# Kernel optimization log

Measured on AMD Instinct MI355X. Metric: run time of the kernel, lower is better.

Reference implementation:

```python
import jax, jax.numpy as jnp
import numpy as np
from jax import lax

NUM_ITER = 20
EPS = 1e-8

# Sobel stencils (match torch grad_x / grad_y exactly)
SX = jnp.array([[-1., 0., 1.], [-2., 0., 2.], [-1., 0., 1.]], jnp.float32)
SY = jnp.array([[-1., -2., -1.], [0., 0., 0.], [1., 2., 1.]], jnp.float32)


def _conv(x, w, groups=1):
    # x: [B,C,H,W], w: [O, C//groups, kh, kw]; cross-correlation, SAME pad (= torch Conv2d padding=1)
    return lax.conv_general_dilated(x, w, (1, 1), 'SAME',
                                    feature_group_count=groups,
                                    dimension_numbers=('NCHW', 'OIHW', 'NCHW'))


def setup_inputs() -> dict:
    key = jax.random.key(0)
    k1, = jax.random.split(key, 1)
    x = jax.random.uniform(k1, (4, 2, 256, 256), dtype=jnp.float32)
    return {
        'x': x,
        'lambda_': jnp.array([0.15], jnp.float32),
        'tau': jnp.array([0.25], jnp.float32),
        'theta': jnp.array([0.3], jnp.float32),
    }


def reference(x, lambda_, tau, theta):
    B, _, H, W = x.shape
    grad_w = jnp.stack([SX, SY])[:, None]            # [2,1,3,3] -> 2-channel image gradient
    sx_dw = jnp.broadcast_to(SX, (2, 1, 3, 3))       # depthwise Sobel-x on 2-channel p
    sy_dw = jnp.broadcast_to(SY, (2, 1, 3, 3))       # depthwise Sobel-y on 2-channel p

    im1 = x[:, 1:2]                                  # [B,1,H,W]
    rho_c = im1 - x[:, 0:1]                          # temporal difference
    grad_im = _conv(im1, grad_w)                     # [B,2,H,W] spatial gradient of frame 1
    norm_grad = jnp.sum(grad_im * grad_im, axis=1, keepdims=True) + EPS  # [B,1,H,W]

    r = tau / theta                                  # [1]
    zeros = jnp.zeros((B, 2, H, W), x.dtype)

    def step(carry, _):
        u, p1, p2 = carry
        rho = rho_c + jnp.sum(grad_im * u, axis=1, keepdims=True)
        th = theta * lambda_ * norm_grad
        # thresholding step (TV-L1 data term prox)
        v = u - jnp.where(jnp.abs(rho) < th,
                          rho / norm_grad,
                          theta * lambda_ * jnp.sign(rho)) * grad_im
        # u update with divergence-like term (original uses 3x3 Sobel gradx/grady on p)
        u = v + theta * (_conv(p1, sx_dw, groups=2) + _conv(p2, sy_dw, groups=2))
        gradu1 = _conv(u[:, 0:1], grad_w)            # [B,2,H,W]
        gradu2 = _conv(u[:, 1:2], grad_w)
        p1 = (p1 + r * gradu1) / (1.0 + r * jnp.sum(jnp.abs(gradu1), axis=1, keepdims=True))
        p2 = (p2 + r * gradu2) / (1.0 + r * jnp.sum(jnp.abs(gradu2), axis=1, keepdims=True))
        return (u, p1, p2), None

    (u, _, _), _ = lax.scan(step, (zeros, zeros, zeros), None, length=NUM_ITER)
    return u
```

## Files before the change

### kernel.cpp

```cpp
#include <hip/hip_runtime.h>

#define HH 256
#define WW 256
#define BB 4
#define HW (HH*WW)
#define N_ITER 20
#define EPSV 1e-8f

#define FUSE 4
#define TILE 32
#define HALO (2*FUSE)
#define EXT  (TILE + 2*HALO)
#define EPAD 49
#define NTHR 768
#define RPS  3

__device__ __forceinline__ float ldz(const float* __restrict__ p, int y, int x) {
    if ((unsigned)y < HH && (unsigned)x < WW) return p[y*WW + x];
    return 0.0f;
}

template<int FIRST, int LAST>
__global__ __launch_bounds__(NTHR)
void tvl1_fused(const float* __restrict__ xin,
                float* __restrict__ u,
                float* __restrict__ p1, float* __restrict__ p2,
                float* __restrict__ gxc, float* __restrict__ gyc,
                float* __restrict__ rcc,
                const float* __restrict__ lam, const float* __restrict__ tau,
                const float* __restrict__ the) {
    __shared__ float4 su[EXT][EPAD];
    __shared__ float4 sp[EXT][EPAD];

    const int tid = threadIdx.x;
    const int sx  = tid % EXT;
    const int sy3 = (tid / EXT) * RPS;
    const int b  = blockIdx.z;
    const int ox = blockIdx.x*TILE - HALO;
    const int oy = blockIdx.y*TILE - HALO;
    const int pb = b*2*HW, cb = b*HW;
    const float theta = the[0];
    const float tl = theta * lam[0];
    const float r = tau[0] / theta;

    const int gxx = ox + sx;
    const bool inx = ((unsigned)gxx < WW);

    float ru0[RPS], ru1[RPS], rp10[RPS], rp11[RPS], rp20[RPS], rp21[RPS];
    float rgx[RPS], rgy[RPS], rrc[RPS];
    bool updr[RPS];

    const int rT = (sy3 == 0) ? 0 : sy3 - 1;
    const int rB = (sy3 + RPS >= EXT) ? EXT-1 : sy3 + RPS;
    const int xm = (sx == 0) ? 0 : sx - 1;
    const int xp = (sx == EXT-1) ? EXT-1 : sx + 1;

    #pragma unroll
    for (int j = 0; j < RPS; ++j) {
        int ry = sy3 + j;
        int gyy = oy + ry;
        bool img = inx && ((unsigned)gyy < HH);
        updr[j] = img && (ry >= 1) && (ry < EXT-1) && (sx >= 1) && (sx < EXT-1);
    }

    if (FIRST) {
        float im1r[RPS], im0r[RPS];
        #pragma unroll
        for (int j = 0; j < RPS; ++j) {
            int gyy = oy + sy3 + j;
            im1r[j] = ldz(xin + pb + HW, gyy, gxx);
            im0r[j] = ldz(xin + pb,      gyy, gxx);
            su[sy3 + j][sx] = make_float4(im1r[j], im0r[j], 0.f, 0.f);
        }
        __syncthreads();
        {
            float4 Vm[RPS+2], Vc[RPS+2], Vp[RPS+2];
            Vm[0] = su[rT][xm];     Vc[0] = su[rT][sx];   Vp[0] = su[rT][xp];
            Vm[1] = su[sy3  ][xm];                        Vp[1] = su[sy3  ][xp];
            Vm[2] = su[sy3+1][xm];                        Vp[2] = su[sy3+1][xp];
            Vm[3] = su[sy3+2][xm];                        Vp[3] = su[sy3+2][xp];
            Vm[4] = su[rB][xm];     Vc[4] = su[rB][sx];   Vp[4] = su[rB][xp];
            Vc[1] = make_float4(im1r[0], im0r[0], 0.f, 0.f);
            Vc[2] = make_float4(im1r[1], im0r[1], 0.f, 0.f);
            Vc[3] = make_float4(im1r[2], im0r[2], 0.f, 0.f);
            #pragma unroll
            for (int j = 0; j < RPS; ++j) {
                rgx[j] = (Vp[j].x-Vm[j].x) + 2.f*(Vp[j+1].x-Vm[j+1].x) + (Vp[j+2].x-Vm[j+2].x);
                rgy[j] = (Vm[j+2].x-Vm[j].x) + 2.f*(Vc[j+2].x-Vc[j].x) + (Vp[j+2].x-Vp[j].x);
                rrc[j] = im1r[j] - im0r[j];
                ru0[j]=0.f; ru1[j]=0.f;
                rp10[j]=0.f; rp11[j]=0.f; rp20[j]=0.f; rp21[j]=0.f;
                int ry = sy3 + j;
                if (ry >= HALO && ry < HALO+TILE && sx >= HALO && sx < HALO+TILE) {
                    int gi = (oy + ry)*WW + gxx;
                    gxc[cb + gi] = rgx[j];
                    gyc[cb + gi] = rgy[j];
                    rcc[cb + gi] = rrc[j];
                }
            }
        }
        __syncthreads();
        #pragma unroll
        for (int j = 0; j < RPS; ++j) {
            su[sy3 + j][sx] = make_float4(0.f, 0.f, 0.f, 0.f);
            sp[sy3 + j][sx] = make_float4(0.f, 0.f, 0.f, 0.f);
        }
        __syncthreads();
    } else {
        #pragma unroll
        for (int j = 0; j < RPS; ++j) {
            int ry = sy3 + j;
            int gyy = oy + ry;
            bool img = inx && ((unsigned)gyy < HH);
            float v0=0.f,v1=0.f,w0=0.f,w1=0.f,w2=0.f,w3=0.f,a=0.f,c=0.f,d=0.f;
            if (img) {
                int gi = gyy*WW + gxx;
                v0 = u[pb + gi];   v1 = u[pb + HW + gi];
                w0 = p1[pb + gi];  w1 = p1[pb + HW + gi];
                w2 = p2[pb + gi];  w3 = p2[pb + HW + gi];
                a  = gxc[cb + gi]; c  = gyc[cb + gi];  d = rcc[cb + gi];
            }
            ru0[j]=v0; ru1[j]=v1; rp10[j]=w0; rp11[j]=w1; rp20[j]=w2; rp21[j]=w3;
            rgx[j]=a; rgy[j]=c; rrc[j]=d;
            su[ry][sx] = make_float4(v0, v1, 0.f, 0.f);
            sp[ry][sx] = make_float4(w0, w1, w2, w3);
        }
        __syncthreads();
    }

    #pragma unroll
    for (int it = 0; it < FUSE; ++it) {
        {
            float4 Wm[RPS+2], Wc[RPS+2], Wp[RPS+2];
            Wm[0] = sp[rT][xm];     Wc[0] = sp[rT][sx];   Wp[0] = sp[rT][xp];
            Wm[1] = sp[sy3  ][xm];                        Wp[1] = sp[sy3  ][xp];
            Wm[2] = sp[sy3+1][xm];                        Wp[2] = sp[sy3+1][xp];
            Wm[3] = sp[sy3+2][xm];                        Wp[3] = sp[sy3+2][xp];
            Wm[4] = sp[rB][xm];     Wc[4] = sp[rB][sx];   Wp[4] = sp[rB][xp];
            Wc[1] = make_float4(rp10[0], rp11[0], rp20[0], rp21[0]);
            Wc[2] = make_float4(rp10[1], rp11[1], rp20[1], rp21[1]);
            Wc[3] = make_float4(rp10[2], rp11[2], rp20[2], rp21[2]);
            #pragma unroll
            for (int j = 0; j < RPS; ++j) {
                if (updr[j]) {
                    float x0 = (Wp[j].x-Wm[j].x) + 2.f*(Wp[j+1].x-Wm[j+1].x) + (Wp[j+2].x-Wm[j+2].x);
                    float x1 = (Wp[j].y-Wm[j].y) + 2.f*(Wp[j+1].y-Wm[j+1].y) + (Wp[j+2].y-Wm[j+2].y);
                    float y0 = (Wm[j+2].z-Wm[j].z) + 2.f*(Wc[j+2].z-Wc[j].z) + (Wp[j+2].z-Wp[j].z);
                    float y1 = (Wm[j+2].w-Wm[j].w) + 2.f*(Wc[j+2].w-Wc[j].w) + (Wp[j+2].w-Wp[j].w);

                    float g_x = rgx[j], g_y = rgy[j];
                    float ng  = g_x*g_x + g_y*g_y + EPSV;
                    float rho = rrc[j] + g_x*ru0[j] + g_y*ru1[j];
                    float th  = tl * ng;
                    float sgn = (rho > 0.f) ? 1.f : ((rho < 0.f) ? -1.f : 0.f);
                    float dd  = (fabsf(rho) < th) ? (rho / ng) : (tl * sgn);
                    ru0[j] = ru0[j] - dd*g_x + theta*(x0 + y0);
                    ru1[j] = ru1[j] - dd*g_y + theta*(x1 + y1);
                    su[sy3+j][sx] = make_float4(ru0[j], ru1[j], 0.f, 0.f);
                }
            }
        }
        __syncthreads();

        if (LAST && it == FUSE-1) break;

        {
            float4 Vm[RPS+2], Vc[RPS+2], Vp[RPS+2];
            Vm[0] = su[rT][xm];     Vc[0] = su[rT][sx];   Vp[0] = su[rT][xp];
            Vm[1] = su[sy3  ][xm];                        Vp[1] = su[sy3  ][xp];
            Vm[2] = su[sy3+1][xm];                        Vp[2] = su[sy3+1][xp];
            Vm[3] = su[sy3+2][xm];                        Vp[3] = su[sy3+2][xp];
            Vm[4] = su[rB][xm];     Vc[4] = su[rB][sx];   Vp[4] = su[rB][xp];
            Vc[1] = make_float4(ru0[0], ru1[0], 0.f, 0.f);
            Vc[2] = make_float4(ru0[1], ru1[1], 0.f, 0.f);
            Vc[3] = make_float4(ru0[2], ru1[2], 0.f, 0.f);
            #pragma unroll
            for (int j = 0; j < RPS; ++j) {
                if (updr[j]) {
                    float g1x = (Vp[j].x-Vm[j].x) + 2.f*(Vp[j+1].x-Vm[j+1].x) + (Vp[j+2].x-Vm[j+2].x);
                    float g1y = (Vm[j+2].x-Vm[j].x) + 2.f*(Vc[j+2].x-Vc[j].x) + (Vp[j+2].x-Vp[j].x);
                    float g2x = (Vp[j].y-Vm[j].y) + 2.f*(Vp[j+1].y-Vm[j+1].y) + (Vp[j+2].y-Vm[j+2].y);
                    float g2y = (Vm[j+2].y-Vm[j].y) + 2.f*(Vc[j+2].y-Vc[j].y) + (Vp[j+2].y-Vp[j].y);
                    float inv1 = 1.f / (1.f + r*(fabsf(g1x) + fabsf(g1y)));
                    float inv2 = 1.f / (1.f + r*(fabsf(g2x) + fabsf(g2y)));
                    rp10[j] = (rp10[j] + r*g1x) * inv1;
                    rp11[j] = (rp11[j] + r*g1y) * inv1;
                    rp20[j] = (rp20[j] + r*g2x) * inv2;
                    rp21[j] = (rp21[j] + r*g2y) * inv2;
                    sp[sy3+j][sx] = make_float4(rp10[j], rp11[j], rp20[j], rp21[j]);
                }
            }
        }
        __syncthreads();
    }

    #pragma unroll
    for (int j = 0; j < RPS; ++j) {
        int ry = sy3 + j;
        if (updr[j] && ry >= HALO && ry < HALO+TILE && sx >= HALO && sx < HALO+TILE) {
            int go = (oy + ry)*WW + (ox + sx);
            u[pb + go]      = ru0[j];
            u[pb + HW + go] = ru1[j];
            if (!LAST) {
                p1[pb + go]      = rp10[j];
                p1[pb + HW + go] = rp11[j];
                p2[pb + go]      = rp20[j];
                p2[pb + HW + go] = rp21[j];
            }
        }
    }
}

extern "C" void kernel_launch(void* const* d_in, const int* in_sizes, int n_in,
                              void* d_out, int out_size, void* d_ws, size_t ws_size,
                              hipStream_t stream) {
    const float* xin = (const float*)d_in[0];
    const float* lam = (const float*)d_in[1];
    const float* tau = (const float*)d_in[2];
    const float* the = (const float*)d_in[3];
    float* u = (float*)d_out;

    float* ws = (float*)d_ws;
    float* p1 = ws;
    float* p2 = ws + (size_t)BB*2*HW;
    float* gx = ws + (size_t)2*BB*2*HW;
    float* gy = gx + (size_t)BB*HW;
    float* rc = gy + (size_t)BB*HW;

    dim3 blk(NTHR, 1, 1);
    dim3 grd(WW/TILE, HH/TILE, BB);
    tvl1_fused<1,0><<<grd, blk, 0, stream>>>(xin, u, p1, p2, gx, gy, rc, lam, tau, the);
    tvl1_fused<0,0><<<grd, blk, 0, stream>>>(xin, u, p1, p2, gx, gy, rc, lam, tau, the);
    tvl1_fused<0,0><<<grd, blk, 0, stream>>>(xin, u, p1, p2, gx, gy, rc, lam, tau, the);
    tvl1_fused<0,0><<<grd, blk, 0, stream>>>(xin, u, p1, p2, gx, gy, rc, lam, tau, the);
    tvl1_fused<0,1><<<grd, blk, 0, stream>>>(xin, u, p1, p2, gx, gy, rc, lam, tau, the);
}
```

Measured before the change: 91.15 us.

## Replace five kernel launches with one cooperative persistent kernel using grid sync

Measured after the change: 244.2 us. 168% more time.

```diff
diff --git a/kernel.cpp b/kernel.cpp
--- a/kernel.cpp
+++ b/kernel.cpp
@@ -1,4 +1,7 @@
 #include <hip/hip_runtime.h>
+#include <hip/hip_cooperative_groups.h>
+
+namespace cg = cooperative_groups;
 
 #define HH 256
 #define WW 256
@@ -8,6 +11,7 @@
 #define EPSV 1e-8f
 
 #define FUSE 4
+#define NPH  5
 #define TILE 32
 #define HALO (2*FUSE)
 #define EXT  (TILE + 2*HALO)
@@ -20,15 +24,14 @@
     return 0.0f;
 }
 
-template<int FIRST, int LAST>
 __global__ __launch_bounds__(NTHR)
-void tvl1_fused(const float* __restrict__ xin,
-                float* __restrict__ u,
-                float* __restrict__ p1, float* __restrict__ p2,
-                float* __restrict__ gxc, float* __restrict__ gyc,
-                float* __restrict__ rcc,
-                const float* __restrict__ lam, const float* __restrict__ tau,
-                const float* __restrict__ the) {
+void tvl1_persist(const float* __restrict__ xin,
+                  float* __restrict__ u,
+                  float* __restrict__ p1, float* __restrict__ p2,
+                  const float* __restrict__ lam, const float* __restrict__ tau,
+                  const float* __restrict__ the) {
+    cg::grid_group gridg = cg::this_grid();
+
     __shared__ float4 su[EXT][EPAD];
     __shared__ float4 sp[EXT][EPAD];
 
@@ -38,7 +41,7 @@
     const int b  = blockIdx.z;
     const int ox = blockIdx.x*TILE - HALO;
     const int oy = blockIdx.y*TILE - HALO;
-    const int pb = b*2*HW, cb = b*HW;
+    const int pb = b*2*HW;
     const float theta = the[0];
     const float tl = theta * lam[0];
     const float r = tau[0] / theta;
@@ -58,12 +61,11 @@
     #pragma unroll
     for (int j = 0; j < RPS; ++j) {
         int ry = sy3 + j;
-        int gyy = oy + ry;
-        bool img = inx && ((unsigned)gyy < HH);
+        bool img = inx && ((unsigned)(oy + ry) < HH);
         updr[j] = img && (ry >= 1) && (ry < EXT-1) && (sx >= 1) && (sx < EXT-1);
     }
 
-    if (FIRST) {
+    {
         float im1r[RPS], im0r[RPS];
         #pragma unroll
         for (int j = 0; j < RPS; ++j) {
@@ -73,141 +75,138 @@
             su[sy3 + j][sx] = make_float4(im1r[j], im0r[j], 0.f, 0.f);
         }
         __syncthreads();
-        {
-            float4 Vm[RPS+2], Vc[RPS+2], Vp[RPS+2];
-            Vm[0] = su[rT][xm];     Vc[0] = su[rT][sx];   Vp[0] = su[rT][xp];
-            Vm[1] = su[sy3  ][xm];                        Vp[1] = su[sy3  ][xp];
-            Vm[2] = su[sy3+1][xm];                        Vp[2] = su[sy3+1][xp];
-            Vm[3] = su[sy3+2][xm];                        Vp[3] = su[sy3+2][xp];
-            Vm[4] = su[rB][xm];     Vc[4] = su[rB][sx];   Vp[4] = su[rB][xp];
-            Vc[1] = make_float4(im1r[0], im0r[0], 0.f, 0.f);
-            Vc[2] = make_float4(im1r[1], im0r[1], 0.f, 0.f);
-            Vc[3] = make_float4(im1r[2], im0r[2], 0.f, 0.f);
+        float4 Vm[RPS+2], Vc[RPS+2], Vp[RPS+2];
+        Vm[0] = su[rT][xm];     Vc[0] = su[rT][sx];   Vp[0] = su[rT][xp];
+        Vm[1] = su[sy3  ][xm];                        Vp[1] = su[sy3  ][xp];
+        Vm[2] = su[sy3+1][xm];                        Vp[2] = su[sy3+1][xp];
+        Vm[3] = su[sy3+2][xm];                        Vp[3] = su[sy3+2][xp];
+        Vm[4] = su[rB][xm];     Vc[4] = su[rB][sx];   Vp[4] = su[rB][xp];
+        Vc[1] = make_float4(im1r[0], im0r[0], 0.f, 0.f);
+        Vc[2] = make_float4(im1r[1], im0r[1], 0.f, 0.f);
+        Vc[3] = make_float4(im1r[2], im0r[2], 0.f, 0.f);
+        #pragma unroll
+        for (int j = 0; j < RPS; ++j) {
+            rgx[j] = (Vp[j].x-Vm[j].x) + 2.f*(Vp[j+1].x-Vm[j+1].x) + (Vp[j+2].x-Vm[j+2].x);
+            rgy[j] = (Vm[j+2].x-Vm[j].x) + 2.f*(Vc[j+2].x-Vc[j].x) + (Vp[j+2].x-Vp[j].x);
+            rrc[j] = im1r[j] - im0r[j];
+            ru0[j]=0.f; ru1[j]=0.f;
+            rp10[j]=0.f; rp11[j]=0.f; rp20[j]=0.f; rp21[j]=0.f;
+        }
+        __syncthreads();
+        #pragma unroll
+        for (int j = 0; j < RPS; ++j) {
+            su[sy3 + j][sx] = make_float4(0.f, 0.f, 0.f, 0.f);
+            sp[sy3 + j][sx] = make_float4(0.f, 0.f, 0.f, 0.f);
+        }
+        __syncthreads();
+    }
+
+    for (int ph = 0; ph < NPH; ++ph) {
+        const bool last = (ph == NPH-1);
+
+        if (ph > 0) {
             #pragma unroll
             for (int j = 0; j < RPS; ++j) {
-                rgx[j] = (Vp[j].x-Vm[j].x) + 2.f*(Vp[j+1].x-Vm[j+1].x) + (Vp[j+2].x-Vm[j+2].x);
-                rgy[j] = (Vm[j+2].x-Vm[j].x) + 2.f*(Vc[j+2].x-Vc[j].x) + (Vp[j+2].x-Vp[j].x);
-                rrc[j] = im1r[j] - im0r[j];
-                ru0[j]=0.f; ru1[j]=0.f;
-                rp10[j]=0.f; rp11[j]=0.f; rp20[j]=0.f; rp21[j]=0.f;
                 int ry = sy3 + j;
-                if (ry >= HALO && ry < HALO+TILE && sx >= HALO && sx < HALO+TILE) {
-                    int gi = (oy + ry)*WW + gxx;
-                    gxc[cb + gi] = rgx[j];
-                    gyc[cb + gi] = rgy[j];
-                    rcc[cb + gi] = rrc[j];
-                }
-            }
-        }
-        __syncthreads();
-        #pragma unroll
-        for (int j = 0; j < RPS; ++j) {
-            su[sy3 + j][sx] = make_float4(0.f, 0.f, 0.f, 0.f);
-            sp[sy3 + j][sx] = make_float4(0.f, 0.f, 0.f, 0.f);
-        }
-        __syncthreads();
-    } else {
+                int gyy = oy + ry;
+                bool img = inx && ((unsigned)gyy < HH);
+                float v0=0.f,v1=0.f,w0=0.f,w1=0.f,w2=0.f,w3=0.f;
+                if (img) {
+                    int gi = gyy*WW + gxx;
+                    v0 = u[pb + gi];   v1 = u[pb + HW + gi];
+                    w0 = p1[pb + gi];  w1 = p1[pb + HW + gi];
+                    w2 = p2[pb + gi];  w3 = p2[pb + HW + gi];
+                }
+                ru0[j]=v0; ru1[j]=v1; rp10[j]=w0; rp11[j]=w1; rp20[j]=w2; rp21[j]=w3;
+                su[ry][sx] = make_float4(v0, v1, 0.f, 0.f);
+                sp[ry][sx] = make_float4(w0, w1, w2, w3);
+            }
+            __syncthreads();
+        }
+
+        #pragma unroll
+        for (int it = 0; it < FUSE; ++it) {
+            {
+                float4 Wm[RPS+2], Wc[RPS+2], Wp[RPS+2];
+                Wm[0] = sp[rT][xm];     Wc[0] = sp[rT][sx];   Wp[0] = sp[rT][xp];
+                Wm[1] = sp[sy3  ][xm];                        Wp[1] = sp[sy3  ][xp];
+                Wm[2] = sp[sy3+1][xm];                        Wp[2] = sp[sy3+1][xp];
+                Wm[3] = sp[sy3+2][xm];                        Wp[3] = sp[sy3+2][xp];
+                Wm[4] = sp[rB][xm];     Wc[4] = sp[rB][sx];   Wp[4] = sp[rB][xp];
+                Wc[1] = make_float4(rp10[0], rp11[0], rp20[0], rp21[0]);
+                Wc[2] = make_float4(rp10[1], rp11[1], rp20[1], rp21[1]);
+                Wc[3] = make_float4(rp10[2], rp11[2], rp20[2], rp21[2]);
+                #pragma unroll
+                for (int j = 0; j < RPS; ++j) {
+                    if (updr[j]) {
+                        float x0 = (Wp[j].x-Wm[j].x) + 2.f*(Wp[j+1].x-Wm[j+1].x) + (Wp[j+2].x-Wm[j+2].x);
+                        float x1 = (Wp[j].y-Wm[j].y) + 2.f*(Wp[j+1].y-Wm[j+1].y) + (Wp[j+2].y-Wm[j+2].y);
+                        float y0 = (Wm[j+2].z-Wm[j].z) + 2.f*(Wc[j+2].z-Wc[j].z) + (Wp[j+2].z-Wp[j].z);
+                        float y1 = (Wm[j+2].w-Wm[j].w) + 2.f*(Wc[j+2].w-Wc[j].w) + (Wp[j+2].w-Wp[j].w);
+
+                        float g_x = rgx[j], g_y = rgy[j];
+                        float ng  = g_x*g_x + g_y*g_y + EPSV;
+                        float rho = rrc[j] + g_x*ru0[j] + g_y*ru1[j];
+                        float th  = tl * ng;
+                        float sgn = (rho > 0.f) ? 1.f : ((rho < 0.f) ? -1.f : 0.f);
+                        float dd  = (fabsf(rho) < th) ? (rho / ng) : (tl * sgn);
+                        ru0[j] = ru0[j] - dd*g_x + theta*(x0 + y0);
+                        ru1[j] = ru1[j] - dd*g_y + theta*(x1 + y1);
+                        su[sy3+j][sx] = make_float4(ru0[j], ru1[j], 0.f, 0.f);
+                    }
+                }
+            }
+            __syncthreads();
+
+            if (last && it == FUSE-1) break;
+
+            {
+                float4 Vm[RPS+2], Vc[RPS+2], Vp[RPS+2];
+                Vm[0] = su[rT][xm];     Vc[0] = su[rT][sx];   Vp[0] = su[rT][xp];
+                Vm[1] = su[sy3  ][xm];                        Vp[1] = su[sy3  ][xp];
+                Vm[2] = su[sy3+1][xm];                        Vp[2] = su[sy3+1][xp];
+                Vm[3] = su[sy3+2][xm];                        Vp[3] = su[sy3+2][xp];
+                Vm[4] = su[rB][xm];     Vc[4] = su[rB][sx];   Vp[4] = su[rB][xp];
+                Vc[1] = make_float4(ru0[0], ru1[0], 0.f, 0.f);
+                Vc[2] = make_float4(ru0[1], ru1[1], 0.f, 0.f);
+                Vc[3] = make_float4(ru0[2], ru1[2], 0.f, 0.f);
+                #pragma unroll
+                for (int j = 0; j < RPS; ++j) {
+                    if (updr[j]) {
+                        float g1x = (Vp[j].x-Vm[j].x) + 2.f*(Vp[j+1].x-Vm[j+1].x) + (Vp[j+2].x-Vm[j+2].x);
+                        float g1y = (Vm[j+2].x-Vm[j].x) + 2.f*(Vc[j+2].x-Vc[j].x) + (Vp[j+2].x-Vp[j].x);
+                        float g2x = (Vp[j].y-Vm[j].y) + 2.f*(Vp[j+1].y-Vm[j+1].y) + (Vp[j+2].y-Vm[j+2].y);
+                        float g2y = (Vm[j+2].y-Vm[j].y) + 2.f*(Vc[j+2].y-Vc[j].y) + (Vp[j+2].y-Vp[j].y);
+                        float inv1 = 1.f / (1.f + r*(fabsf(g1x) + fabsf(g1y)));
+                        float inv2 = 1.f / (1.f + r*(fabsf(g2x) + fabsf(g2y)));
+                        rp10[j] = (rp10[j] + r*g1x) * inv1;
+                        rp11[j] = (rp11[j] + r*g1y) * inv1;
+                        rp20[j] = (rp20[j] + r*g2x) * inv2;
+                        rp21[j] = (rp21[j] + r*g2y) * inv2;
+                        sp[sy3+j][sx] = make_float4(rp10[j], rp11[j], rp20[j], rp21[j]);
+                    }
+                }
+            }
+            __syncthreads();
+        }
+
         #pragma unroll
         for (int j = 0; j < RPS; ++j) {
             int ry = sy3 + j;
-            int gyy = oy + ry;
-            bool img = inx && ((unsigned)gyy < HH);
-            float v0=0.f,v1=0.f,w0=0.f,w1=0.f,w2=0.f,w3=0.f,a=0.f,c=0.f,d=0.f;
-            if (img) {
-                int gi = gyy*WW + gxx;
-                v0 = u[pb + gi];   v1 = u[pb + HW + gi];
-                w0 = p1[pb + gi];  w1 = p1[pb + HW + gi];
-                w2 = p2[pb + gi];  w3 = p2[pb + HW + gi];
-                a  = gxc[cb + gi]; c  = gyc[cb + gi];  d = rcc[cb + gi];
-            }
-            ru0[j]=v0; ru1[j]=v1; rp10[j]=w0; rp11[j]=w1; rp20[j]=w2; rp21[j]=w3;
-            rgx[j]=a; rgy[j]=c; rrc[j]=d;
-            su[ry][sx] = make_float4(v0, v1, 0.f, 0.f);
-            sp[ry][sx] = make_float4(w0, w1, w2, w3);
-        }
-        __syncthreads();
-    }
-
-    #pragma unroll
-    for (int it = 0; it < FUSE; ++it) {
-        {
-            float4 Wm[RPS+2], Wc[RPS+2], Wp[RPS+2];
-            Wm[0] = sp[rT][xm];     Wc[0] = sp[rT][sx];   Wp[0] = sp[rT][xp];
-            Wm[1] = sp[sy3  ][xm];                        Wp[1] = sp[sy3  ][xp];
-            Wm[2] = sp[sy3+1][xm];                        Wp[2] = sp[sy3+1][xp];
-            Wm[3] = sp[sy3+2][xm];                        Wp[3] = sp[sy3+2][xp];
-            Wm[4] = sp[rB][xm];     Wc[4] = sp[rB][sx];   Wp[4] = sp[rB][xp];
-            Wc[1] = make_float4(rp10[0], rp11[0], rp20[0], rp21[0]);
-            Wc[2] = make_float4(rp10[1], rp11[1], rp20[1], rp21[1]);
-            Wc[3] = make_float4(rp10[2], rp11[2], rp20[2], rp21[2]);
-            #pragma unroll
-            for (int j = 0; j < RPS; ++j) {
-                if (updr[j]) {
-                    float x0 = (Wp[j].x-Wm[j].x) + 2.f*(Wp[j+1].x-Wm[j+1].x) + (Wp[j+2].x-Wm[j+2].x);
-                    float x1 = (Wp[j].y-Wm[j].y) + 2.f*(Wp[j+1].y-Wm[j+1].y) + (Wp[j+2].y-Wm[j+2].y);
-                    float y0 = (Wm[j+2].z-Wm[j].z) + 2.f*(Wc[j+2].z-Wc[j].z) + (Wp[j+2].z-Wp[j].z);
-                    float y1 = (Wm[j+2].w-Wm[j].w) + 2.f*(Wc[j+2].w-Wc[j].w) + (Wp[j+2].w-Wp[j].w);
-
-                    float g_x = rgx[j], g_y = rgy[j];
-                    float ng  = g_x*g_x + g_y*g_y + EPSV;
-                    float rho = rrc[j] + g_x*ru0[j] + g_y*ru1[j];
-                    float th  = tl * ng;
-                    float sgn = (rho > 0.f) ? 1.f : ((rho < 0.f) ? -1.f : 0.f);
-                    float dd  = (fabsf(rho) < th) ? (rho / ng) : (tl * sgn);
-                    ru0[j] = ru0[j] - dd*g_x + theta*(x0 + y0);
-                    ru1[j] = ru1[j] - dd*g_y + theta*(x1 + y1);
-                    su[sy3+j][sx] = make_float4(ru0[j], ru1[j], 0.f, 0.f);
-                }
-            }
-        }
-        __syncthreads();
-
-        if (LAST && it == FUSE-1) break;
-
-        {
-            float4 Vm[RPS+2], Vc[RPS+2], Vp[RPS+2];
-            Vm[0] = su[rT][xm];     Vc[0] = su[rT][sx];   Vp[0] = su[rT][xp];
-            Vm[1] = su[sy3  ][xm];                        Vp[1] = su[sy3  ][xp];
-            Vm[2] = su[sy3+1][xm];                        Vp[2] = su[sy3+1][xp];
-            Vm[3] = su[sy3+2][xm];                        Vp[3] = su[sy3+2][xp];
-            Vm[4] = su[rB][xm];     Vc[4] = su[rB][sx];   Vp[4] = su[rB][xp];
-            Vc[1] = make_float4(ru0[0], ru1[0], 0.f, 0.f);
-            Vc[2] = make_float4(ru0[1], ru1[1], 0.f, 0.f);
-            Vc[3] = make_float4(ru0[2], ru1[2], 0.f, 0.f);
-            #pragma unroll
-            for (int j = 0; j < RPS; ++j) {
-                if (updr[j]) {
-                    float g1x = (Vp[j].x-Vm[j].x) + 2.f*(Vp[j+1].x-Vm[j+1].x) + (Vp[j+2].x-Vm[j+2].x);
-                    float g1y = (Vm[j+2].x-Vm[j].x) + 2.f*(Vc[j+2].x-Vc[j].x) + (Vp[j+2].x-Vp[j].x);
-                    float g2x = (Vp[j].y-Vm[j].y) + 2.f*(Vp[j+1].y-Vm[j+1].y) + (Vp[j+2].y-Vm[j+2].y);
-                    float g2y = (Vm[j+2].y-Vm[j].y) + 2.f*(Vc[j+2].y-Vc[j].y) + (Vp[j+2].y-Vp[j].y);
-                    float inv1 = 1.f / (1.f + r*(fabsf(g1x) + fabsf(g1y)));
-                    float inv2 = 1.f / (1.f + r*(fabsf(g2x) + fabsf(g2y)));
-                    rp10[j] = (rp10[j] + r*g1x) * inv1;
-                    rp11[j] = (rp11[j] + r*g1y) * inv1;
-                    rp20[j] = (rp20[j] + r*g2x) * inv2;
-                    rp21[j] = (rp21[j] + r*g2y) * inv2;
-                    sp[sy3+j][sx] = make_float4(rp10[j], rp11[j], rp20[j], rp21[j]);
-                }
-            }
-        }
-        __syncthreads();
-    }
-
-    #pragma unroll
-    for (int j = 0; j < RPS; ++j) {
-        int ry = sy3 + j;
-        if (updr[j] && ry >= HALO && ry < HALO+TILE && sx >= HALO && sx < HALO+TILE) {
-            int go = (oy + ry)*WW + (ox + sx);
-            u[pb + go]      = ru0[j];
-            u[pb + HW + go] = ru1[j];
-            if (!LAST) {
-                p1[pb + go]      = rp10[j];
-                p1[pb + HW + go] = rp11[j];
-                p2[pb + go]      = rp20[j];
-                p2[pb + HW + go] = rp21[j];
-            }
-        }
+            if (updr[j] && ry >= HALO && ry < HALO+TILE && sx >= HALO && sx < HALO+TILE) {
+                int go = (oy + ry)*WW + (ox + sx);
+                u[pb + go]      = ru0[j];
+                u[pb + HW + go] = ru1[j];
+                if (!last) {
+                    p1[pb + go]      = rp10[j];
+                    p1[pb + HW + go] = rp11[j];
+                    p2[pb + go]      = rp20[j];
+                    p2[pb + HW + go] = rp21[j];
+                }
+            }
+        }
+
+        if (!last) gridg.sync();
     }
 }
 
@@ -223,15 +222,11 @@
     float* ws = (float*)d_ws;
     float* p1 = ws;
     float* p2 = ws + (size_t)BB*2*HW;
-    float* gx = ws + (size_t)2*BB*2*HW;
-    float* gy = gx + (size_t)BB*HW;
-    float* rc = gy + (size_t)BB*HW;
 
     dim3 blk(NTHR, 1, 1);
     dim3 grd(WW/TILE, HH/TILE, BB);
-    tvl1_fused<1,0><<<grd, blk, 0, stream>>>(xin, u, p1, p2, gx, gy, rc, lam, tau, the);
-    tvl1_fused<0,0><<<grd, blk, 0, stream>>>(xin, u, p1, p2, gx, gy, rc, lam, tau, the);
-    tvl1_fused<0,0><<<grd, blk, 0, stream>>>(xin, u, p1, p2, gx, gy, rc, lam, tau, the);
-    tvl1_fused<0,0><<<grd, blk, 0, stream>>>(xin, u, p1, p2, gx, gy, rc, lam, tau, the);
-    tvl1_fused<0,1><<<grd, blk, 0, stream>>>(xin, u, p1, p2, gx, gy, rc, lam, tau, the);
+    void* args[] = { (void*)&xin, (void*)&u, (void*)&p1, (void*)&p2,
+                     (void*)&lam, (void*)&tau, (void*)&the };
+    hipLaunchCooperativeKernel(reinterpret_cast<void*>(tvl1_persist),
+                               grd, blk, args, 0, stream);
 }
```
